# Kernel optimization log

Measured on AMD Instinct MI355X. Metric: run time of the kernel, lower is better.

Reference implementation:

```python
import jax, jax.numpy as jnp
import numpy as np

WS = (7, 7, 7)
NUM_HEADS = 16
DIM = 512
HEAD_DIM = DIM // NUM_HEADS
SCALE = HEAD_DIM ** (-0.5)


def _rel_index():
    # Swin-3D relative position index, computed statically with numpy.
    coords = np.stack(np.meshgrid(np.arange(WS[0]), np.arange(WS[1]), np.arange(WS[2]), indexing='ij'))
    coords = coords.reshape(3, -1)                       # [3, n]
    rel = coords[:, :, None] - coords[:, None, :]        # [3, n, n]
    rel = rel.transpose(1, 2, 0).astype(np.int64)        # [n, n, 3]
    rel[..., 0] += WS[0] - 1
    rel[..., 1] += WS[1] - 1
    rel[..., 2] += WS[2] - 1
    rel[..., 0] *= (2 * WS[1] - 1) * (2 * WS[2] - 1)
    rel[..., 1] *= 2 * WS[2] - 1
    return rel.sum(-1)                                   # [n, n]

REL_INDEX = jnp.asarray(_rel_index(), dtype=jnp.int32)


def setup_inputs() -> dict:
    key = jax.random.key(0)
    ks = jax.random.split(key, 6)
    B, nw = 2, 64
    b, n, c = B * nw, WS[0] * WS[1] * WS[2], DIM  # 128, 343, 512
    x = jax.random.normal(ks[0], (b, n, c), jnp.float32)
    q_global = jax.random.normal(ks[1], (B, 1, NUM_HEADS, n, HEAD_DIM), jnp.float32)
    mask = jax.random.normal(ks[2], (nw, n, n), jnp.float32)
    kv_w = jax.random.normal(ks[3], (2 * c, c), jnp.float32) * (c ** -0.5)
    proj_w = jax.random.normal(ks[4], (c, c), jnp.float32) * (c ** -0.5)
    proj_b = jnp.zeros((c,), jnp.float32)
    num_rel = (2 * WS[0] - 1) * (2 * WS[1] - 1) * (2 * WS[2] - 1)  # 2197
    rpb_table = jax.random.normal(ks[5], (num_rel, NUM_HEADS), jnp.float32) * 0.02
    return {"x": x, "D": 7, "H": 7, "W": 7, "mask": mask, "q_global": q_global,
            "kv_w": kv_w, "proj_w": proj_w, "proj_b": proj_b, "rpb_table": rpb_table}


def reference(x, D, H, W, mask, q_global, kv_w, proj_w, proj_b, rpb_table):
    b, n, c = x.shape
    h, hd = NUM_HEADS, c // NUM_HEADS
    B = q_global.shape[0]
    # q_global [B,1,h,n,hd] repeated over windows -> [b,h,n,hd]
    q = jnp.broadcast_to(q_global, (B, b // B, h, n, hd)).reshape(b, h, n, hd) * SCALE
    kv = (x @ kv_w.T).reshape(b, n, 2, h, hd).transpose(2, 0, 3, 1, 4)  # [2,b,h,n,hd]
    k, v = kv[0], kv[1]
    attn = jnp.einsum('bhnd,bhmd->bhnm', q, k)  # [b,h,n,n]
    bias = rpb_table[REL_INDEX[:n, :n].reshape(-1)].reshape(n, n, h).transpose(2, 0, 1)
    attn = attn + bias[None]
    nw = mask.shape[0]
    attn = (attn.reshape(b // nw, nw, h, n, n) + mask[None, :, None]).reshape(b, h, n, n)
    attn = jax.nn.softmax(attn, axis=-1)
    out = jnp.einsum('bhnm,bhmd->bhnd', attn, v).transpose(0, 2, 1, 3).reshape(b, n, c)
    return out @ proj_w.T + proj_b
```

## Files before the change

kernel.cpp:

```cpp
#include <hip/hip_runtime.h>

typedef __bf16 bf16x8 __attribute__((ext_vector_type(8)));
typedef __bf16 bf16x2 __attribute__((ext_vector_type(2)));
typedef float f32x4 __attribute__((ext_vector_type(4)));
typedef unsigned u32x4v __attribute__((ext_vector_type(4)));

#define MFMA16(a, b, c) __builtin_amdgcn_mfma_f32_16x16x32_bf16(a, b, c, 0, 0, 0)
#define LOG2E 1.4426950408889634f

typedef __attribute__((address_space(3))) void lds_void;
typedef __attribute__((address_space(1))) const void gbl_void;
__device__ inline void glds16(const __bf16* g, __bf16* l) {
  __builtin_amdgcn_global_load_lds((gbl_void*)g, (lds_void*)l, 16, 0, 0);
}

__device__ inline float blo(unsigned u) { return __builtin_bit_cast(float, u << 16); }
__device__ inline float bhi(unsigned u) { return __builtin_bit_cast(float, u & 0xffff0000u); }
__device__ inline unsigned pk2(float a, float b) {
  bf16x2 t; t[0] = (__bf16)a; t[1] = (__bf16)b;
  return __builtin_bit_cast(unsigned, t);
}

__global__ void cvt_scale(const float* __restrict__ src, __bf16* __restrict__ dst,
                          int n8, float scale) {
  int i = blockIdx.x * blockDim.x + threadIdx.x;
  if (i >= n8) return;
  const float4* p = (const float4*)(src + i * 8);
  float4 a = p[0], b = p[1];
  bf16x8 r;
  r[0] = (__bf16)(a.x * scale); r[1] = (__bf16)(a.y * scale);
  r[2] = (__bf16)(a.z * scale); r[3] = (__bf16)(a.w * scale);
  r[4] = (__bf16)(b.x * scale); r[5] = (__bf16)(b.y * scale);
  r[6] = (__bf16)(b.z * scale); r[7] = (__bf16)(b.w * scale);
  *(bf16x8*)(dst + i * 8) = r;
}

__global__ void pack_bias(const float* __restrict__ rpb, __bf16* __restrict__ dst) {
  int i = blockIdx.x * blockDim.x + threadIdx.x;
  if (i >= 16 * 15488) return;
  int h = i / 15488, rem = i % 15488;
  int qt = rem / 704, rem2 = rem % 704;
  int tp = rem2 >> 6, lane = rem2 & 63;
  int quad = lane >> 4, l15 = lane & 15;
  int q = qt * 16 + l15;
  bf16x8 v;
#pragma unroll
  for (int t2 = 0; t2 < 2; t2++)
#pragma unroll
    for (int r = 0; r < 4; r++) {
      int kc = tp * 32 + quad * 8 + t2 * 4 + r;
      float val = -1e30f;
      if (q < 343 && kc < 343) {
        int q0 = q / 49, q1 = (q / 7) % 7, q2 = q % 7;
        int k0 = kc / 49, k1 = (kc / 7) % 7, k2 = kc % 7;
        int idx = ((q0 - k0 + 6) * 13 + (q1 - k1 + 6)) * 13 + (q2 - k2 + 6);
        val = rpb[idx * 16 + h] * LOG2E;
      }
      v[t2 * 4 + r] = (__bf16)val;
    }
  *(bf16x8*)(dst + i * 8) = v;
}

__global__ void pack_mask(const float* __restrict__ mask, __bf16* __restrict__ dst) {
  int i = blockIdx.x * blockDim.x + threadIdx.x;
  if (i >= 64 * 15488) return;
  int w = i / 15488, rem = i % 15488;
  int qt = rem / 704, rem2 = rem % 704;
  int tp = rem2 >> 6, lane = rem2 & 63;
  int quad = lane >> 4, l15 = lane & 15;
  int q = qt * 16 + l15;
  const float* s = mask + w * 117649;
  bf16x8 v;
#pragma unroll
  for (int t2 = 0; t2 < 2; t2++)
#pragma unroll
    for (int r = 0; r < 4; r++) {
      int kc = tp * 32 + quad * 8 + t2 * 4 + r;
      float val = (q < 343 && kc < 343) ? s[q * 343 + kc] * LOG2E : -1e30f;
      v[t2 * 4 + r] = (__bf16)val;
    }
  *(bf16x8*)(dst + i * 8) = v;
}

template <int MODE>
__global__ void __launch_bounds__(256, 2)
gemm_async(const __bf16* __restrict__ A, const __bf16* __restrict__ B, const int K,
           void* __restrict__ out0, void* __restrict__ out1,
           const float* __restrict__ pbias) {
  __shared__ __bf16 As[128 * 32];
  __shared__ __bf16 Bs[128 * 32];
  const int tid = threadIdx.x;
  const int lane = tid & 63, wave = tid >> 6;
  const int quad = lane >> 4, l15 = lane & 15;
  const int wm = wave >> 1, wn = wave & 1;
  const int m0 = blockIdx.y * 128, n0 = blockIdx.x * 128;
  const int sr = lane >> 2, sc = (lane & 3) * 8;
  const __bf16* Ab = A + (m0 + wave * 16 + sr) * K + sc;
  const __bf16* Bb = B + (n0 + wave * 16 + sr) * K + sc;
  __bf16* Asl = As + wave * 512;
  __bf16* Bsl = Bs + wave * 512;
  f32x4 acc[4][4] = {};
  for (int k0 = 0; k0 < K; k0 += 32) {
    glds16(Ab + k0, Asl);
    glds16(Ab + 64 * K + k0, Asl + 2048);
    glds16(Bb + k0, Bsl);
    glds16(Bb + 64 * K + k0, Bsl + 2048);
    __syncthreads();
    bf16x8 af[4], bfr[4];
#pragma unroll
    for (int i = 0; i < 4; i++) {
      af[i] = *(const bf16x8*)(As + (wm * 64 + i * 16 + l15) * 32 + quad * 8);
      bfr[i] = *(const bf16x8*)(Bs + (wn * 64 + i * 16 + l15) * 32 + quad * 8);
    }
#pragma unroll
    for (int i = 0; i < 4; i++)
#pragma unroll
      for (int j = 0; j < 4; j++)
        acc[i][j] = MFMA16(af[i], bfr[j], acc[i][j]);
    __syncthreads();
  }
#pragma unroll
  for (int i = 0; i < 4; i++) {
    const int rowb = m0 + wm * 64 + i * 16 + quad * 4;
#pragma unroll
    for (int r = 0; r < 4; r++) {
      const int row = rowb + r;
      if constexpr (MODE == 0) {
        const int bb = row / 343, pos = row % 343;
#pragma unroll
        for (int j = 0; j < 4; j++) {
          const int col = n0 + wn * 64 + j * 16 + l15;
          const int two = col >> 9, hh = (col >> 5) & 15, d = col & 31;
          __bf16* dst = two ? (__bf16*)out1 : (__bf16*)out0;
          dst[((bb * 16 + hh) * 343 + pos) * 32 + d] = (__bf16)acc[i][j][r];
        }
      } else {
        float* o = (float*)out0;
#pragma unroll
        for (int j = 0; j < 4; j++) {
          const int col = n0 + wn * 64 + j * 16 + l15;
          o[row * 512 + col] = acc[i][j][r] + pbias[col];
        }
      }
    }
  }
}

__global__ void __launch_bounds__(512, 2)
attn_win(const __bf16* __restrict__ qs, const __bf16* __restrict__ kk,
         const __bf16* __restrict__ vv, const __bf16* __restrict__ bias_pk,
         const __bf16* __restrict__ mask_pk, __bf16* __restrict__ ao) {
  __shared__ __bf16 Ks[352 * 40];
  __shared__ __bf16 Vt[32 * 360];
  const int bh = blockIdx.x;
  const int b = bh >> 4, h = bh & 15;
  const int tid = threadIdx.x;
  const int lane = tid & 63, wave = tid >> 6;
  const int quad = lane >> 4, l15 = lane & 15;
  const __bf16* ksrc = kk + (b * 16 + h) * 10976;
  const __bf16* vsrc = vv + (b * 16 + h) * 10976;
  for (int i = tid; i < 352 * 4; i += 512) {
    const int row = i >> 2, seg = (i & 3) * 8;
    bf16x8 val;
    if (row < 343) {
      val = *(const bf16x8*)(ksrc + row * 32 + seg);
    } else {
#pragma unroll
      for (int e = 0; e < 8; e++) val[e] = (__bf16)0.f;
    }
    *(bf16x8*)(Ks + row * 40 + seg) = val;
  }
  Vt[(tid >> 4) * 360 + 343 + (tid & 15)] = (__bf16)0.f;
  for (int i = tid; i < 1372; i += 512) {
    const int pos = i >> 2, seg = (i & 3) * 8;
    bf16x8 v = *(const bf16x8*)(vsrc + pos * 32 + seg);
#pragma unroll
    for (int e = 0; e < 8; e++) Vt[(seg + e) * 360 + pos] = v[e];
  }

  const int b2 = b >> 6, w = b & 63;
  const __bf16* qbase = qs + (b2 * 16 + h) * 10976;
  const __bf16* bpk = bias_pk + h * 123904;
  const __bf16* mpk = mask_pk + w * 123904;
  const int nqt = (wave < 6) ? 3 : 2;

  bf16x8 aq[3];
#pragma unroll
  for (int t = 0; t < 3; t++) {
    int qt = wave + 8 * t; if (qt > 21) qt = 21;
    const int arow = qt * 16 + l15;
    const int arowc = arow < 343 ? arow : 342;
    aq[t] = *(const bf16x8*)(qbase + arowc * 32 + quad * 8);
  }
  bf16x8 ones;
  {
    const __bf16 ov = (l15 == 0) ? (__bf16)1.f : (__bf16)0.f;
#pragma unroll
    for (int e = 0; e < 8; e++) ones[e] = ov;
  }
  const int krow = (l15 >> 2) * 8 + (l15 & 3);
  __syncthreads();

  f32x4 o0[3], o1[3], o2[3];
#pragma unroll
  for (int t = 0; t < 3; t++)
#pragma unroll
    for (int r = 0; r < 4; r++) { o0[t][r] = 0.f; o1[t][r] = 0.f; o2[t][r] = 0.f; }

  for (int c = 0; c < 11; c++) {
    const bf16x8 bk0 = *(const bf16x8*)(Ks + (c * 32 + krow) * 40 + quad * 8);
    const bf16x8 bk1 = *(const bf16x8*)(Ks + (c * 32 + krow + 4) * 40 + quad * 8);
    const bf16x8 bv0 = *(const bf16x8*)(Vt + l15 * 360 + c * 32 + quad * 8);
    const bf16x8 bv1 = *(const bf16x8*)(Vt + (16 + l15) * 360 + c * 32 + quad * 8);
    const __bf16* bq = bpk + c * 512 + lane * 8;
    const __bf16* mq = mpk + c * 512 + lane * 8;
#pragma unroll
    for (int t = 0; t < 3; t++) {
      if (t >= nqt) break;
      const int qoff = (wave + 8 * t) * 5632;
      const uint4 bu = *(const uint4*)(bq + qoff);
      const uint4 mu = *(const uint4*)(mq + qoff);
      f32x4 s0, s1;
      s0[0] = blo(bu.x) + blo(mu.x); s0[1] = bhi(bu.x) + bhi(mu.x);
      s0[2] = blo(bu.y) + blo(mu.y); s0[3] = bhi(bu.y) + bhi(mu.y);
      s1[0] = blo(bu.z) + blo(mu.z); s1[1] = bhi(bu.z) + bhi(mu.z);
      s1[2] = blo(bu.w) + blo(mu.w); s1[3] = bhi(bu.w) + bhi(mu.w);
      s0 = MFMA16(bk0, aq[t], s0);
      s1 = MFMA16(bk1, aq[t], s1);
#pragma unroll
      for (int r = 0; r < 4; r++) {
        s0[r] = __builtin_amdgcn_exp2f(s0[r]);
        s1[r] = __builtin_amdgcn_exp2f(s1[r]);
      }
      u32x4v uv;
      uv[0] = pk2(s0[0], s0[1]); uv[1] = pk2(s0[2], s0[3]);
      uv[2] = pk2(s1[0], s1[1]); uv[3] = pk2(s1[2], s1[3]);
      const bf16x8 ap = __builtin_bit_cast(bf16x8, uv);
      o0[t] = MFMA16(ap, bv0, o0[t]);
      o1[t] = MFMA16(ap, bv1, o1[t]);
      o2[t] = MFMA16(ap, ones, o2[t]);
    }
  }

#pragma unroll
  for (int t = 0; t < 3; t++) {
    if (t >= nqt) break;
    const int qt = wave + 8 * t;
#pragma unroll
    for (int r = 0; r < 4; r++) {
      const float lsum = __shfl(o2[t][r], lane & 48);
      const float inv = __builtin_amdgcn_rcpf(lsum);
      const int row = qt * 16 + quad * 4 + r;
      if (row < 343) {
        __bf16* op = ao + (b * 343 + row) * 512 + h * 32;
        op[l15] = (__bf16)(o0[t][r] * inv);
        op[16 + l15] = (__bf16)(o1[t][r] * inv);
      }
    }
  }
}

extern "C" void kernel_launch(void* const* d_in, const int* in_sizes, int n_in,
                              void* d_out, int out_size, void* d_ws, size_t ws_size,
                              hipStream_t stream) {
  (void)in_sizes; (void)n_in; (void)out_size; (void)ws_size;
  const float* x      = (const float*)d_in[0];
  const float* mask   = (const float*)d_in[4];
  const float* qg     = (const float*)d_in[5];
  const float* kv_w   = (const float*)d_in[6];
  const float* proj_w = (const float*)d_in[7];
  const float* proj_b = (const float*)d_in[8];
  const float* rpb    = (const float*)d_in[9];

  char* ws = (char*)d_ws;
  __bf16* q_bf    = (__bf16*)(ws);
  __bf16* bias_pk = (__bf16*)(ws + 702464);
  __bf16* mask_pk = (__bf16*)(ws + 4667392);
  __bf16* kvw_b   = (__bf16*)(ws + 20527104);
  __bf16* projw_b = (__bf16*)(ws + 21575680);
  __bf16* kb      = (__bf16*)(ws + 22099968);
  __bf16* vb      = (__bf16*)(ws + 67057664);
  __bf16* xb      = (__bf16*)(ws + 112015360);
  __bf16* aob     = (__bf16*)(ws + 112015360);

  const float QSCALE = 0.17677669529663687f * LOG2E;

  cvt_scale<<<172, 256, 0, stream>>>(qg, q_bf, 43904, QSCALE);
  cvt_scale<<<10976, 256, 0, stream>>>(x, xb, 2809856, 1.f);
  cvt_scale<<<256, 256, 0, stream>>>(kv_w, kvw_b, 65536, 1.f);
  cvt_scale<<<128, 256, 0, stream>>>(proj_w, projw_b, 32768, 1.f);
  pack_bias<<<968, 256, 0, stream>>>(rpb, bias_pk);
  pack_mask<<<3872, 256, 0, stream>>>(mask, mask_pk);
  gemm_async<0><<<dim3(8, 343), 256, 0, stream>>>(xb, kvw_b, 512, kb, vb, nullptr);
  attn_win<<<2048, 512, 0, stream>>>(q_bf, kb, vb, bias_pk, mask_pk, aob);
  gemm_async<1><<<dim3(4, 343), 256, 0, stream>>>(aob, projw_b, 512, d_out, nullptr, proj_b);
}
```

Measured before the change: 414.2 us.

## Fuse x conversion into GEMM, MFMA-based bias/mask add, XCD-aware block remap

Drops the standalone fp32-to-bf16 conversion of x by loading fp32 directly in the KV GEMM and converting in registers before the LDS store. The bias and mask tables are repacked so that half the lanes read bias and half read mask; an identity-matrix MFMA then sums them into the score accumulator instead of doing scalar bf16 unpack-and-add. Both the GEMMs and the attention kernel remap block IDs to group work per XCD for L2 locality. The attention kernel also gains s_setprio around its compute and a higher occupancy hint. In exchange, the A operand of the KV GEMM now goes through registers instead of async direct-to-LDS loads, and each score tile costs extra MFMAs.

```diff
diff --git a/kernel.cpp b/kernel.cpp
--- a/kernel.cpp
+++ b/kernel.cpp
@@ -14,8 +14,6 @@
   __builtin_amdgcn_global_load_lds((gbl_void*)g, (lds_void*)l, 16, 0, 0);
 }
 
-__device__ inline float blo(unsigned u) { return __builtin_bit_cast(float, u << 16); }
-__device__ inline float bhi(unsigned u) { return __builtin_bit_cast(float, u & 0xffff0000u); }
 __device__ inline unsigned pk2(float a, float b) {
   bf16x2 t; t[0] = (__bf16)a; t[1] = (__bf16)b;
   return __builtin_bit_cast(unsigned, t);
@@ -40,24 +38,22 @@
   if (i >= 16 * 15488) return;
   int h = i / 15488, rem = i % 15488;
   int qt = rem / 704, rem2 = rem % 704;
-  int tp = rem2 >> 6, lane = rem2 & 63;
-  int quad = lane >> 4, l15 = lane & 15;
-  int q = qt * 16 + l15;
+  int c = rem2 / 64, rem3 = rem2 % 64;
+  int half = rem3 >> 5, qd = (rem3 >> 4) & 1, l15 = rem3 & 15;
+  int key = c * 32 + (l15 >> 2) * 8 + (l15 & 3) + half * 4;
   bf16x8 v;
 #pragma unroll
-  for (int t2 = 0; t2 < 2; t2++)
-#pragma unroll
-    for (int r = 0; r < 4; r++) {
-      int kc = tp * 32 + quad * 8 + t2 * 4 + r;
-      float val = -1e30f;
-      if (q < 343 && kc < 343) {
-        int q0 = q / 49, q1 = (q / 7) % 7, q2 = q % 7;
-        int k0 = kc / 49, k1 = (kc / 7) % 7, k2 = kc % 7;
-        int idx = ((q0 - k0 + 6) * 13 + (q1 - k1 + 6)) * 13 + (q2 - k2 + 6);
-        val = rpb[idx * 16 + h] * LOG2E;
-      }
-      v[t2 * 4 + r] = (__bf16)val;
-    }
+  for (int e = 0; e < 8; e++) {
+    int q = qt * 16 + qd * 8 + e;
+    float val = -1e30f;
+    if (q < 343 && key < 343) {
+      int q0 = q / 49, q1 = (q / 7) % 7, q2 = q % 7;
+      int k0 = key / 49, k1 = (key / 7) % 7, k2 = key % 7;
+      int idx = ((q0 - k0 + 6) * 13 + (q1 - k1 + 6)) * 13 + (q2 - k2 + 6);
+      val = rpb[idx * 16 + h] * LOG2E;
+    }
+    v[e] = (__bf16)val;
+  }
   *(bf16x8*)(dst + i * 8) = v;
 }
 
@@ -66,25 +62,23 @@
   if (i >= 64 * 15488) return;
   int w = i / 15488, rem = i % 15488;
   int qt = rem / 704, rem2 = rem % 704;
-  int tp = rem2 >> 6, lane = rem2 & 63;
-  int quad = lane >> 4, l15 = lane & 15;
-  int q = qt * 16 + l15;
+  int c = rem2 / 64, rem3 = rem2 % 64;
+  int half = rem3 >> 5, qd = (rem3 >> 4) & 1, l15 = rem3 & 15;
+  int key = c * 32 + (l15 >> 2) * 8 + (l15 & 3) + half * 4;
   const float* s = mask + w * 117649;
   bf16x8 v;
 #pragma unroll
-  for (int t2 = 0; t2 < 2; t2++)
-#pragma unroll
-    for (int r = 0; r < 4; r++) {
-      int kc = tp * 32 + quad * 8 + t2 * 4 + r;
-      float val = (q < 343 && kc < 343) ? s[q * 343 + kc] * LOG2E : -1e30f;
-      v[t2 * 4 + r] = (__bf16)val;
-    }
+  for (int e = 0; e < 8; e++) {
+    int q = qt * 16 + qd * 8 + e;
+    float val = (q < 343 && key < 343) ? s[q * 343 + key] * LOG2E : -1e30f;
+    v[e] = (__bf16)val;
+  }
   *(bf16x8*)(dst + i * 8) = v;
 }
 
 template <int MODE>
 __global__ void __launch_bounds__(256, 2)
-gemm_async(const __bf16* __restrict__ A, const __bf16* __restrict__ B, const int K,
+gemm_async(const void* __restrict__ Araw, const __bf16* __restrict__ B, const int K,
            void* __restrict__ out0, void* __restrict__ out1,
            const float* __restrict__ pbias) {
   __shared__ __bf16 As[128 * 32];
@@ -93,16 +87,40 @@
   const int lane = tid & 63, wave = tid >> 6;
   const int quad = lane >> 4, l15 = lane & 15;
   const int wm = wave >> 1, wn = wave & 1;
-  const int m0 = blockIdx.y * 128, n0 = blockIdx.x * 128;
+  const int nwg = gridDim.x * gridDim.y;
+  int bid = blockIdx.y * gridDim.x + blockIdx.x;
+  {
+    const int xcd = bid & 7, idx = bid >> 3, qq = nwg >> 3, rr = nwg & 7;
+    bid = (xcd < rr ? xcd * (qq + 1) : rr * (qq + 1) + (xcd - rr) * qq) + idx;
+  }
+  const int m0 = (bid / gridDim.x) * 128, n0 = (bid % gridDim.x) * 128;
   const int sr = lane >> 2, sc = (lane & 3) * 8;
-  const __bf16* Ab = A + (m0 + wave * 16 + sr) * K + sc;
   const __bf16* Bb = B + (n0 + wave * 16 + sr) * K + sc;
+  __bf16* Bsl = Bs + wave * 512;
+  const __bf16* Ab = nullptr; const float* Af = nullptr;
   __bf16* Asl = As + wave * 512;
-  __bf16* Bsl = Bs + wave * 512;
+  if constexpr (MODE == 0) {
+    Af = (const float*)Araw + (size_t)(m0 + wave * 16 + sr) * K + sc;
+  } else {
+    Ab = (const __bf16*)Araw + (size_t)(m0 + wave * 16 + sr) * K + sc;
+  }
   f32x4 acc[4][4] = {};
   for (int k0 = 0; k0 < K; k0 += 32) {
-    glds16(Ab + k0, Asl);
-    glds16(Ab + 64 * K + k0, Asl + 2048);
+    if constexpr (MODE == 0) {
+      float4 a0 = *(const float4*)(Af + k0), a1 = *(const float4*)(Af + k0 + 4);
+      float4 b0 = *(const float4*)(Af + (size_t)64 * K + k0);
+      float4 b1 = *(const float4*)(Af + (size_t)64 * K + k0 + 4);
+      bf16x8 c0, c1;
+      c0[0] = (__bf16)a0.x; c0[1] = (__bf16)a0.y; c0[2] = (__bf16)a0.z; c0[3] = (__bf16)a0.w;
+      c0[4] = (__bf16)a1.x; c0[5] = (__bf16)a1.y; c0[6] = (__bf16)a1.z; c0[7] = (__bf16)a1.w;
+      c1[0] = (__bf16)b0.x; c1[1] = (__bf16)b0.y; c1[2] = (__bf16)b0.z; c1[3] = (__bf16)b0.w;
+      c1[4] = (__bf16)b1.x; c1[5] = (__bf16)b1.y; c1[6] = (__bf16)b1.z; c1[7] = (__bf16)b1.w;
+      *(bf16x8*)(As + (wave * 16 + sr) * 32 + sc) = c0;
+      *(bf16x8*)(As + (64 + wave * 16 + sr) * 32 + sc) = c1;
+    } else {
+      glds16(Ab + k0, Asl);
+      glds16(Ab + 64 * K + k0, Asl + 2048);
+    }
     glds16(Bb + k0, Bsl);
     glds16(Bb + 64 * K + k0, Bsl + 2048);
     __syncthreads();
@@ -146,13 +164,14 @@
   }
 }
 
-__global__ void __launch_bounds__(512, 2)
+__global__ void __launch_bounds__(512, 6)
 attn_win(const __bf16* __restrict__ qs, const __bf16* __restrict__ kk,
          const __bf16* __restrict__ vv, const __bf16* __restrict__ bias_pk,
          const __bf16* __restrict__ mask_pk, __bf16* __restrict__ ao) {
   __shared__ __bf16 Ks[352 * 40];
   __shared__ __bf16 Vt[32 * 360];
-  const int bh = blockIdx.x;
+  const int bid = blockIdx.x;
+  const int bh = (bid & 7) * 256 + (bid >> 3);
   const int b = bh >> 4, h = bh & 15;
   const int tid = threadIdx.x;
   const int lane = tid & 63, wave = tid >> 6;
@@ -180,8 +199,8 @@
 
   const int b2 = b >> 6, w = b & 63;
   const __bf16* qbase = qs + (b2 * 16 + h) * 10976;
-  const __bf16* bpk = bias_pk + h * 123904;
-  const __bf16* mpk = mask_pk + w * 123904;
+  const __bf16* tab = (quad < 2 ? bias_pk + h * 123904 : mask_pk + w * 123904)
+                      + (quad & 1) * 128 + l15 * 8;
   const int nqt = (wave < 6) ? 3 : 2;
 
   bf16x8 aq[3];
@@ -193,10 +212,14 @@
     aq[t] = *(const bf16x8*)(qbase + arowc * 32 + quad * 8);
   }
   bf16x8 ones;
+  bf16x8 idf;
   {
     const __bf16 ov = (l15 == 0) ? (__bf16)1.f : (__bf16)0.f;
 #pragma unroll
-    for (int e = 0; e < 8; e++) ones[e] = ov;
+    for (int e = 0; e < 8; e++) {
+      ones[e] = ov;
+      idf[e] = ((quad & 1) * 8 + e == l15) ? (__bf16)1.f : (__bf16)0.f;
+    }
   }
   const int krow = (l15 >> 2) * 8 + (l15 & 3);
   __syncthreads();
@@ -212,19 +235,17 @@
     const bf16x8 bk1 = *(const bf16x8*)(Ks + (c * 32 + krow + 4) * 40 + quad * 8);
     const bf16x8 bv0 = *(const bf16x8*)(Vt + l15 * 360 + c * 32 + quad * 8);
     const bf16x8 bv1 = *(const bf16x8*)(Vt + (16 + l15) * 360 + c * 32 + quad * 8);
-    const __bf16* bq = bpk + c * 512 + lane * 8;
-    const __bf16* mq = mpk + c * 512 + lane * 8;
 #pragma unroll
     for (int t = 0; t < 3; t++) {
       if (t >= nqt) break;
-      const int qoff = (wave + 8 * t) * 5632;
-      const uint4 bu = *(const uint4*)(bq + qoff);
-      const uint4 mu = *(const uint4*)(mq + qoff);
-      f32x4 s0, s1;
-      s0[0] = blo(bu.x) + blo(mu.x); s0[1] = bhi(bu.x) + bhi(mu.x);
-      s0[2] = blo(bu.y) + blo(mu.y); s0[3] = bhi(bu.y) + bhi(mu.y);
-      s1[0] = blo(bu.z) + blo(mu.z); s1[1] = bhi(bu.z) + bhi(mu.z);
-      s1[2] = blo(bu.w) + blo(mu.w); s1[3] = bhi(bu.w) + bhi(mu.w);
+      const int qt = wave + 8 * t;
+      const __bf16* tb = tab + (qt * 11 + c) * 512;
+      const bf16x8 f0 = *(const bf16x8*)tb;
+      const bf16x8 f1 = *(const bf16x8*)(tb + 256);
+      const f32x4 z = {0.f, 0.f, 0.f, 0.f};
+      __builtin_amdgcn_s_setprio(1);
+      f32x4 s0 = MFMA16(f0, idf, z);
+      f32x4 s1 = MFMA16(f1, idf, z);
       s0 = MFMA16(bk0, aq[t], s0);
       s1 = MFMA16(bk1, aq[t], s1);
 #pragma unroll
@@ -239,6 +260,7 @@
       o0[t] = MFMA16(ap, bv0, o0[t]);
       o1[t] = MFMA16(ap, bv1, o1[t]);
       o2[t] = MFMA16(ap, ones, o2[t]);
+      __builtin_amdgcn_s_setprio(0);
     }
   }
 
@@ -280,18 +302,16 @@
   __bf16* projw_b = (__bf16*)(ws + 21575680);
   __bf16* kb      = (__bf16*)(ws + 22099968);
   __bf16* vb      = (__bf16*)(ws + 67057664);
-  __bf16* xb      = (__bf16*)(ws + 112015360);
   __bf16* aob     = (__bf16*)(ws + 112015360);
 
   const float QSCALE = 0.17677669529663687f * LOG2E;
 
   cvt_scale<<<172, 256, 0, stream>>>(qg, q_bf, 43904, QSCALE);
-  cvt_scale<<<10976, 256, 0, stream>>>(x, xb, 2809856, 1.f);
   cvt_scale<<<256, 256, 0, stream>>>(kv_w, kvw_b, 65536, 1.f);
   cvt_scale<<<128, 256, 0, stream>>>(proj_w, projw_b, 32768, 1.f);
   pack_bias<<<968, 256, 0, stream>>>(rpb, bias_pk);
   pack_mask<<<3872, 256, 0, stream>>>(mask, mask_pk);
-  gemm_async<0><<<dim3(8, 343), 256, 0, stream>>>(xb, kvw_b, 512, kb, vb, nullptr);
+  gemm_async<0><<<dim3(8, 343), 256, 0, stream>>>(x, kvw_b, 512, kb, vb, nullptr);
   attn_win<<<2048, 512, 0, stream>>>(q_bf, kb, vb, bias_pk, mask_pk, aob);
   gemm_async<1><<<dim3(4, 343), 256, 0, stream>>>(aob, projw_b, 512, d_out, nullptr, proj_b);
 }
```

New measurement: 539.3 us. 1.3x slower.
